# Kernel optimization log

Measured on AMD Instinct MI355X. Metric: run time of the kernel, lower is better.

Reference implementation:

```python
import jax, jax.numpy as jnp
import numpy as np

RANK_WEIGHT = 0.1  # init kwarg rank_weight
EPS = 1e-08


def setup_inputs() -> dict:
    key = jax.random.key(0)
    k1, k2, k3, k4 = jax.random.split(key, 4)
    B, D = 8192, 128
    return {
        "q_embeddings": jax.random.normal(k1, (B, D), dtype=jnp.float32),
        "a_embeddings": jax.random.normal(k2, (B, D), dtype=jnp.float32),
        "question_ids": jax.random.randint(k3, (B,), 0, 2048, dtype=jnp.int64),
        "ranks": jax.random.uniform(k4, (B,), dtype=jnp.float32),
    }


def reference(q_embeddings, a_embeddings, question_ids, ranks):
    # NOTE: the original computes q@a.T/temperature into `similarity` but the
    # per-sample loop recomputes sims WITHOUT temperature; we match the loop math.
    sims = jnp.matmul(q_embeddings, a_embeddings.T)  # [B, B]
    same_q = question_ids[:, None] == question_ids[None, :]  # [B, B] bool
    # pos_mask weight per positive column j: 1 - rank_weight * ranks[j]
    w = jnp.where(same_q, 1.0 - RANK_WEIGHT * ranks[None, :], 0.0)  # [B, B]
    # stable exp-ratio: sum(w*exp(s)) / sum(exp(s))
    m = jnp.max(sims, axis=1, keepdims=True)
    e = jnp.exp(sims - m)
    num = jnp.sum(w * e, axis=1)
    den = jnp.sum(e, axis=1)
    loss = jnp.mean(-jnp.log(num / den + EPS))
    pred = jnp.argmax(sims, axis=1)  # [B]
    correct = jnp.take_along_axis(w, pred[:, None], axis=1)[:, 0] > 0
    accuracy = jnp.mean(correct.astype(jnp.float32))
    return loss, accuracy
```

## Files before the change

### kernel.cpp

```cpp
#include <hip/hip_runtime.h>
#include <hip/hip_bf16.h>
#include <cmath>

#define B_N 8192
#define D_K 128
#define CSPLIT 8
#define T_ITERS 16

typedef short bf16x8 __attribute__((ext_vector_type(8)));
typedef unsigned short u16x8 __attribute__((ext_vector_type(8)));
typedef float f32x4  __attribute__((ext_vector_type(4)));

__device__ inline unsigned short f2bf(float f) {
    unsigned u = __builtin_bit_cast(unsigned, f);
    u += 0x7fffu + ((u >> 16) & 1u);
    return (unsigned short)(u >> 16);
}

__global__ void cvt_kernel(const float* __restrict__ q, const float* __restrict__ a,
                           unsigned short* __restrict__ qb, unsigned short* __restrict__ ab,
                           float* __restrict__ out) {
    int g = blockIdx.x * blockDim.x + threadIdx.x;
    if (g < 2) out[g] = 0.0f;
    float4 q0 = reinterpret_cast<const float4*>(q)[g * 2];
    float4 q1 = reinterpret_cast<const float4*>(q)[g * 2 + 1];
    u16x8 oq;
    oq[0] = f2bf(q0.x); oq[1] = f2bf(q0.y); oq[2] = f2bf(q0.z); oq[3] = f2bf(q0.w);
    oq[4] = f2bf(q1.x); oq[5] = f2bf(q1.y); oq[6] = f2bf(q1.z); oq[7] = f2bf(q1.w);
    *reinterpret_cast<u16x8*>(qb + (size_t)g * 8) = oq;

    float4 a0 = reinterpret_cast<const float4*>(a)[g * 2];
    float4 a1 = reinterpret_cast<const float4*>(a)[g * 2 + 1];
    u16x8 oa;
    oa[0] = f2bf(a0.x); oa[1] = f2bf(a0.y); oa[2] = f2bf(a0.z); oa[3] = f2bf(a0.w);
    oa[4] = f2bf(a1.x); oa[5] = f2bf(a1.y); oa[6] = f2bf(a1.z); oa[7] = f2bf(a1.w);
    const int col = g >> 4, sq = g & 15, s = sq >> 2, quad = sq & 3;
    const int chunk = ((col >> 4) * 4 + s) * 64 + quad * 16 + (col & 15);
    *reinterpret_cast<u16x8*>(ab + (size_t)chunk * 8) = oa;
}

__launch_bounds__(256, 4)
__global__ void mpl_part_kernel(const unsigned short* __restrict__ qb,
                                const unsigned short* __restrict__ ab,
                                const int* __restrict__ qids,
                                const float* __restrict__ ranks,
                                float* __restrict__ pden, float* __restrict__ pnum,
                                float* __restrict__ pmax, float* __restrict__ pmaxp) {
    const int tid  = threadIdx.x;
    const int lane = tid & 63;
    const int wave = tid >> 6;
    const int rg   = blockIdx.x >> 3;
    const int cs   = blockIdx.x & 7;
    const int rowBase = rg * 32;
    const int quad = lane >> 4;
    const int l15  = lane & 15;

    bf16x8 qfrag[2][4];
    #pragma unroll
    for (int rt = 0; rt < 2; ++rt) {
        const unsigned short* qrow = qb + (size_t)(rowBase + rt * 16 + l15) * D_K + quad * 8;
        #pragma unroll
        for (int s = 0; s < 4; ++s)
            qfrag[rt][s] = *reinterpret_cast<const bf16x8*>(qrow + s * 32);
    }

    int qidrow[2][4];
    #pragma unroll
    for (int rt = 0; rt < 2; ++rt)
        #pragma unroll
        for (int r = 0; r < 4; ++r)
            qidrow[rt][r] = qids[rowBase + rt * 16 + quad * 4 + r];

    float den[2][4], num[2][4], mxv[2][4], mxp[2][4];
    #pragma unroll
    for (int rt = 0; rt < 2; ++rt)
        #pragma unroll
        for (int r = 0; r < 4; ++r) {
            den[rt][r] = 0.f; num[rt][r] = 0.f;
            mxv[rt][r] = -INFINITY; mxp[rt][r] = -INFINITY;
        }

    const float L2E = 1.4426950408889634f;
    const float CB  = 64.0f;

    const int colStart = cs * 1024 + wave * 256;
    const int tileBase = colStart >> 4;

    #pragma unroll 2
    for (int t = 0; t < T_ITERS; ++t) {
        const int c  = colStart + t * 16 + l15;
        const int qc = qids[c];
        const float wc = 1.0f - 0.1f * ranks[c];

        const unsigned short* bbase = ab + ((size_t)(tileBase + t) * 4) * 512 + lane * 8;
        bf16x8 bfrag[4];
        #pragma unroll
        for (int s = 0; s < 4; ++s)
            bfrag[s] = *reinterpret_cast<const bf16x8*>(bbase + s * 512);

        f32x4 acc0 = {0.f, 0.f, 0.f, 0.f};
        f32x4 acc1 = {0.f, 0.f, 0.f, 0.f};
        #pragma unroll
        for (int s = 0; s < 4; ++s) {
            acc0 = __builtin_amdgcn_mfma_f32_16x16x32_bf16(qfrag[0][s], bfrag[s], acc0, 0, 0, 0);
            acc1 = __builtin_amdgcn_mfma_f32_16x16x32_bf16(qfrag[1][s], bfrag[s], acc1, 0, 0, 0);
        }

        #pragma unroll
        for (int r = 0; r < 4; ++r) {
            {
                float sv = acc0[r];
                float e  = __builtin_amdgcn_exp2f(fmaf(sv, L2E, -CB));
                bool pos = (qc == qidrow[0][r]);
                den[0][r] += e;
                num[0][r] = fmaf(pos ? wc : 0.0f, e, num[0][r]);
                mxv[0][r] = fmaxf(mxv[0][r], sv);
                mxp[0][r] = fmaxf(mxp[0][r], pos ? sv : -INFINITY);
            }
            {
                float sv = acc1[r];
                float e  = __builtin_amdgcn_exp2f(fmaf(sv, L2E, -CB));
                bool pos = (qc == qidrow[1][r]);
                den[1][r] += e;
                num[1][r] = fmaf(pos ? wc : 0.0f, e, num[1][r]);
                mxv[1][r] = fmaxf(mxv[1][r], sv);
                mxp[1][r] = fmaxf(mxp[1][r], pos ? sv : -INFINITY);
            }
        }
    }

    #pragma unroll
    for (int m = 1; m <= 8; m <<= 1) {
        #pragma unroll
        for (int rt = 0; rt < 2; ++rt)
            #pragma unroll
            for (int r = 0; r < 4; ++r) {
                den[rt][r] += __shfl_xor(den[rt][r], m, 64);
                num[rt][r] += __shfl_xor(num[rt][r], m, 64);
                mxv[rt][r]  = fmaxf(mxv[rt][r], __shfl_xor(mxv[rt][r], m, 64));
                mxp[rt][r]  = fmaxf(mxp[rt][r], __shfl_xor(mxp[rt][r], m, 64));
            }
    }

    __shared__ float sden[4][32], snum[4][32], smax[4][32], smaxp[4][32];
    if (l15 == 0) {
        #pragma unroll
        for (int rt = 0; rt < 2; ++rt)
            #pragma unroll
            for (int r = 0; r < 4; ++r) {
                int lr = rt * 16 + quad * 4 + r;
                sden[wave][lr]  = den[rt][r];
                snum[wave][lr]  = num[rt][r];
                smax[wave][lr]  = mxv[rt][r];
                smaxp[wave][lr] = mxp[rt][r];
            }
    }
    __syncthreads();

    if (tid < 32) {
        int lr = tid;
        float d = 0.f, n = 0.f, mv = -INFINITY, mp = -INFINITY;
        #pragma unroll
        for (int w = 0; w < 4; ++w) {
            d += sden[w][lr];
            n += snum[w][lr];
            mv = fmaxf(mv, smax[w][lr]);
            mp = fmaxf(mp, smaxp[w][lr]);
        }
        const int row = rowBase + lr;
        pden[cs * B_N + row]  = d;
        pnum[cs * B_N + row]  = n;
        pmax[cs * B_N + row]  = mv;
        pmaxp[cs * B_N + row] = mp;
    }
}

__launch_bounds__(256, 4)
__global__ void fin_kernel(const float* __restrict__ pden, const float* __restrict__ pnum,
                           const float* __restrict__ pmax, const float* __restrict__ pmaxp,
                           float* __restrict__ out) {
    const int r = blockIdx.x * 256 + threadIdx.x;
    float d = 0.f, n = 0.f, mv = -INFINITY, mp = -INFINITY;
    #pragma unroll
    for (int cs = 0; cs < CSPLIT; ++cs) {
        d += pden[cs * B_N + r];
        n += pnum[cs * B_N + r];
        mv = fmaxf(mv, pmax[cs * B_N + r]);
        mp = fmaxf(mp, pmaxp[cs * B_N + r]);
    }
    float lsum = -logf(n / d + 1e-8f);
    float csum = (mp == mv) ? 1.0f : 0.0f;
    #pragma unroll
    for (int m = 1; m <= 32; m <<= 1) {
        lsum += __shfl_xor(lsum, m, 64);
        csum += __shfl_xor(csum, m, 64);
    }
    __shared__ float sl[4], sc[4];
    const int wave = threadIdx.x >> 6;
    if ((threadIdx.x & 63) == 0) { sl[wave] = lsum; sc[wave] = csum; }
    __syncthreads();
    if (threadIdx.x == 0) {
        float L = sl[0] + sl[1] + sl[2] + sl[3];
        float C = sc[0] + sc[1] + sc[2] + sc[3];
        atomicAdd(&out[0], L * (1.0f / B_N));
        atomicAdd(&out[1], C * (1.0f / B_N));
    }
}

extern "C" void kernel_launch(void* const* d_in, const int* in_sizes, int n_in,
                              void* d_out, int out_size, void* d_ws, size_t ws_size,
                              hipStream_t stream) {
    const float* q     = (const float*)d_in[0];
    const float* a     = (const float*)d_in[1];
    const int*   qids  = (const int*)d_in[2];
    const float* ranks = (const float*)d_in[3];
    float* out = (float*)d_out;

    unsigned short* qb = (unsigned short*)d_ws;
    unsigned short* ab = qb + (size_t)B_N * D_K;
    char* p = (char*)(ab + (size_t)B_N * D_K);
    float* pden  = (float*)p;                p += CSPLIT * B_N * sizeof(float);
    float* pnum  = (float*)p;                p += CSPLIT * B_N * sizeof(float);
    float* pmax  = (float*)p;                p += CSPLIT * B_N * sizeof(float);
    float* pmaxp = (float*)p;

    cvt_kernel<<<(B_N * D_K / 8) / 256, 256, 0, stream>>>(q, a, qb, ab, out);
    mpl_part_kernel<<<256 * CSPLIT, 256, 0, stream>>>(qb, ab, qids, ranks, pden, pnum, pmax, pmaxp);
    fin_kernel<<<B_N / 256, 256, 0, stream>>>(pden, pnum, pmax, pmaxp, out);
}
```

Before: 115.0 us.

## Share column tiles across waves via double-buffered LDS with direct global-to-LDS loads

Before, each of the 4 waves handled the same 32 rows and a different set of columns, so every wave fetched its own B fragments straight from global memory. Now each wave owns its own 32 rows (128 rows per block), and all four waves share one 512-column strip. That strip is streamed into LDS in double-buffered 64-column tiles using global_load_lds, so each B tile is fetched once and reused by four waves. The cross-wave LDS reduction is removed, and CSPLIT becomes 16 so the finalize kernel sums more partials. The cost is a block barrier on every tile and 32 KB of LDS per block, which may limit occupancy.

```diff
diff --git a/kernel.cpp b/kernel.cpp
--- a/kernel.cpp
+++ b/kernel.cpp
@@ -4,12 +4,22 @@
 
 #define B_N 8192
 #define D_K 128
-#define CSPLIT 8
-#define T_ITERS 16
+#define ROWS 128
+#define CSPLIT 16
+#define T_OUT 8
 
 typedef short bf16x8 __attribute__((ext_vector_type(8)));
 typedef unsigned short u16x8 __attribute__((ext_vector_type(8)));
 typedef float f32x4  __attribute__((ext_vector_type(4)));
+
+typedef __attribute__((address_space(3))) unsigned int as3_uint;
+typedef __attribute__((address_space(1))) unsigned int as1_uint;
+
+__device__ __forceinline__ void gl_lds16(const void* g, void* l) {
+    __builtin_amdgcn_global_load_lds((const as1_uint*)(uintptr_t)g,
+                                     (as3_uint*)(unsigned int)(uintptr_t)l,
+                                     16, 0, 0);
+}
 
 __device__ inline unsigned short f2bf(float f) {
     unsigned u = __builtin_bit_cast(unsigned, f);
@@ -46,19 +56,22 @@
                                 const float* __restrict__ ranks,
                                 float* __restrict__ pden, float* __restrict__ pnum,
                                 float* __restrict__ pmax, float* __restrict__ pmaxp) {
+    __shared__ unsigned short smem[2 * 8192];
+
     const int tid  = threadIdx.x;
     const int lane = tid & 63;
     const int wave = tid >> 6;
-    const int rg   = blockIdx.x >> 3;
-    const int cs   = blockIdx.x & 7;
-    const int rowBase = rg * 32;
+    const int rg   = blockIdx.x >> 4;
+    const int cs   = blockIdx.x & 15;
+    const int rowBase = rg * ROWS;
+    const int waveRow = rowBase + wave * 32;
     const int quad = lane >> 4;
     const int l15  = lane & 15;
 
     bf16x8 qfrag[2][4];
     #pragma unroll
     for (int rt = 0; rt < 2; ++rt) {
-        const unsigned short* qrow = qb + (size_t)(rowBase + rt * 16 + l15) * D_K + quad * 8;
+        const unsigned short* qrow = qb + (size_t)(waveRow + rt * 16 + l15) * D_K + quad * 8;
         #pragma unroll
         for (int s = 0; s < 4; ++s)
             qfrag[rt][s] = *reinterpret_cast<const bf16x8*>(qrow + s * 32);
@@ -69,7 +82,7 @@
     for (int rt = 0; rt < 2; ++rt)
         #pragma unroll
         for (int r = 0; r < 4; ++r)
-            qidrow[rt][r] = qids[rowBase + rt * 16 + quad * 4 + r];
+            qidrow[rt][r] = qids[waveRow + rt * 16 + quad * 4 + r];
 
     float den[2][4], num[2][4], mxv[2][4], mxp[2][4];
     #pragma unroll
@@ -82,51 +95,65 @@
 
     const float L2E = 1.4426950408889634f;
     const float CB  = 64.0f;
-
-    const int colStart = cs * 1024 + wave * 256;
-    const int tileBase = colStart >> 4;
-
-    #pragma unroll 2
-    for (int t = 0; t < T_ITERS; ++t) {
-        const int c  = colStart + t * 16 + l15;
-        const int qc = qids[c];
-        const float wc = 1.0f - 0.1f * ranks[c];
-
-        const unsigned short* bbase = ab + ((size_t)(tileBase + t) * 4) * 512 + lane * 8;
-        bf16x8 bfrag[4];
-        #pragma unroll
-        for (int s = 0; s < 4; ++s)
-            bfrag[s] = *reinterpret_cast<const bf16x8*>(bbase + s * 512);
-
-        f32x4 acc0 = {0.f, 0.f, 0.f, 0.f};
-        f32x4 acc1 = {0.f, 0.f, 0.f, 0.f};
-        #pragma unroll
-        for (int s = 0; s < 4; ++s) {
-            acc0 = __builtin_amdgcn_mfma_f32_16x16x32_bf16(qfrag[0][s], bfrag[s], acc0, 0, 0, 0);
-            acc1 = __builtin_amdgcn_mfma_f32_16x16x32_bf16(qfrag[1][s], bfrag[s], acc1, 0, 0, 0);
-        }
-
-        #pragma unroll
-        for (int r = 0; r < 4; ++r) {
-            {
-                float sv = acc0[r];
-                float e  = __builtin_amdgcn_exp2f(fmaf(sv, L2E, -CB));
-                bool pos = (qc == qidrow[0][r]);
-                den[0][r] += e;
-                num[0][r] = fmaf(pos ? wc : 0.0f, e, num[0][r]);
-                mxv[0][r] = fmaxf(mxv[0][r], sv);
-                mxp[0][r] = fmaxf(mxp[0][r], pos ? sv : -INFINITY);
-            }
-            {
-                float sv = acc1[r];
-                float e  = __builtin_amdgcn_exp2f(fmaf(sv, L2E, -CB));
-                bool pos = (qc == qidrow[1][r]);
-                den[1][r] += e;
-                num[1][r] = fmaf(pos ? wc : 0.0f, e, num[1][r]);
-                mxv[1][r] = fmaxf(mxv[1][r], sv);
-                mxp[1][r] = fmaxf(mxp[1][r], pos ? sv : -INFINITY);
-            }
-        }
+    const int colStart = cs * 512;
+
+    const char* gstrip = (const char*)ab + (size_t)cs * 32 * 4096;
+    const int   chunk  = wave * 4096;
+
+    #pragma unroll
+    for (int r = 0; r < 4; ++r)
+        gl_lds16(gstrip + chunk + r * 1024 + lane * 16,
+                 (char*)smem + chunk + r * 1024);
+    __syncthreads();
+
+    for (int t = 0; t < T_OUT; ++t) {
+        const int cur = t & 1, nxt = cur ^ 1;
+        if (t + 1 < T_OUT) {
+            const char* gsrc = gstrip + (size_t)(t + 1) * 16384 + chunk;
+            char*       ldst = (char*)smem + nxt * 16384 + chunk;
+            #pragma unroll
+            for (int r = 0; r < 4; ++r)
+                gl_lds16(gsrc + r * 1024 + lane * 16, ldst + r * 1024);
+        }
+
+        const unsigned short* lbase = smem + cur * 8192 + lane * 8;
+        #pragma unroll
+        for (int u = 0; u < 4; ++u) {
+            f32x4 acc0 = {0.f, 0.f, 0.f, 0.f};
+            f32x4 acc1 = {0.f, 0.f, 0.f, 0.f};
+            #pragma unroll
+            for (int s = 0; s < 4; ++s) {
+                bf16x8 bfrag = *reinterpret_cast<const bf16x8*>(lbase + u * 2048 + s * 512);
+                acc0 = __builtin_amdgcn_mfma_f32_16x16x32_bf16(qfrag[0][s], bfrag, acc0, 0, 0, 0);
+                acc1 = __builtin_amdgcn_mfma_f32_16x16x32_bf16(qfrag[1][s], bfrag, acc1, 0, 0, 0);
+            }
+
+            const int c  = colStart + t * 64 + u * 16 + l15;
+            const int qc = qids[c];
+            const float wc = 1.0f - 0.1f * ranks[c];
+            #pragma unroll
+            for (int r = 0; r < 4; ++r) {
+                {
+                    float sv = acc0[r];
+                    float e  = __builtin_amdgcn_exp2f(fmaf(sv, L2E, -CB));
+                    bool pos = (qc == qidrow[0][r]);
+                    den[0][r] += e;
+                    num[0][r] = fmaf(pos ? wc : 0.0f, e, num[0][r]);
+                    mxv[0][r] = fmaxf(mxv[0][r], sv);
+                    mxp[0][r] = fmaxf(mxp[0][r], pos ? sv : -INFINITY);
+                }
+                {
+                    float sv = acc1[r];
+                    float e  = __builtin_amdgcn_exp2f(fmaf(sv, L2E, -CB));
+                    bool pos = (qc == qidrow[1][r]);
+                    den[1][r] += e;
+                    num[1][r] = fmaf(pos ? wc : 0.0f, e, num[1][r]);
+                    mxv[1][r] = fmaxf(mxv[1][r], sv);
+                    mxp[1][r] = fmaxf(mxp[1][r], pos ? sv : -INFINITY);
+                }
+            }
+        }
+        __syncthreads();
     }
 
     #pragma unroll
@@ -142,36 +169,18 @@
             }
     }
 
-    __shared__ float sden[4][32], snum[4][32], smax[4][32], smaxp[4][32];
     if (l15 == 0) {
         #pragma unroll
-        for (int rt = 0; rt < 2; ++rt)
+        for (int rt = 0; rt < 2; ++rt) {
+            const int rb = cs * B_N + waveRow + rt * 16 + quad * 4;
             #pragma unroll
             for (int r = 0; r < 4; ++r) {
-                int lr = rt * 16 + quad * 4 + r;
-                sden[wave][lr]  = den[rt][r];
-                snum[wave][lr]  = num[rt][r];
-                smax[wave][lr]  = mxv[rt][r];
-                smaxp[wave][lr] = mxp[rt][r];
-            }
-    }
-    __syncthreads();
-
-    if (tid < 32) {
-        int lr = tid;
-        float d = 0.f, n = 0.f, mv = -INFINITY, mp = -INFINITY;
-        #pragma unroll
-        for (int w = 0; w < 4; ++w) {
-            d += sden[w][lr];
-            n += snum[w][lr];
-            mv = fmaxf(mv, smax[w][lr]);
-            mp = fmaxf(mp, smaxp[w][lr]);
-        }
-        const int row = rowBase + lr;
-        pden[cs * B_N + row]  = d;
-        pnum[cs * B_N + row]  = n;
-        pmax[cs * B_N + row]  = mv;
-        pmaxp[cs * B_N + row] = mp;
+                pden[rb + r]  = den[rt][r];
+                pnum[rb + r]  = num[rt][r];
+                pmax[rb + r]  = mxv[rt][r];
+                pmaxp[rb + r] = mxp[rt][r];
+            }
+        }
     }
 }
 
@@ -225,6 +234,7 @@
     float* pmaxp = (float*)p;
 
     cvt_kernel<<<(B_N * D_K / 8) / 256, 256, 0, stream>>>(q, a, qb, ab, out);
-    mpl_part_kernel<<<256 * CSPLIT, 256, 0, stream>>>(qb, ab, qids, ranks, pden, pnum, pmax, pmaxp);
+    mpl_part_kernel<<<(B_N / ROWS) * CSPLIT, 256, 0, stream>>>(qb, ab, qids, ranks,
+                                                               pden, pnum, pmax, pmaxp);
     fin_kernel<<<B_N / 256, 256, 0, stream>>>(pden, pnum, pmax, pmaxp, out);
 }
```

Result: slower. 149.6 us (+30.1%).
